# Kernel optimization log

Hardware: AMD Instinct MI355X
Metric: run time of the kernel (lower is better)

The kernel has to match this reference:

```python
import jax, jax.numpy as jnp
import numpy as np

IMAGE_SIZE = 256
NUM_FACES = 4096
NEAR = 0.1
FAR = 100.0
DRAW_BACKSIDE = False
EPS = 1e-8
CHUNK = 128  # faces processed per scan step (memory/compute tradeoff)


def setup_inputs() -> dict:
    key = jax.random.key(0)
    u = jax.random.uniform(key, (1, NUM_FACES, 3, 3), dtype=jnp.float32)  # fill=rand
    xy = u[..., :2] * 2.0 - 1.0          # screen coords in [-1, 1]
    z = u[..., 2:] * 20.0 + 1.0          # depths in [1, 21], inside (near, far)
    # shrink triangles toward their centroid -> realistic small screen-space triangles
    center = jnp.mean(xy, axis=2, keepdims=True)
    xy = center + (xy - center) * 0.15
    faces = jnp.concatenate([xy, z], axis=-1)  # [B, F, 3, 3]
    return {"faces": faces}


def _rasterize(faces):
    """Z-buffer triangle rasterization. Returns (depth_map, face_index_map).
    Matches the CUDA 'safe' kernel: per pixel, loop faces; point-in-triangle via
    same-sign edge functions; perspective-correct depth 1/zp = sum(w_i / z_i);
    keep the closest face with zp in (near, far); -1 where nothing is drawn.
    Faces are scanned in chunks to avoid materializing [B, F, S, S]."""
    B, F = faces.shape[0], faces.shape[1]
    S = IMAGE_SIZE
    ax = jnp.arange(S, dtype=jnp.float32)
    # pixel centers in normalized coords: p = (2*i + 1 - S) / S
    yp = (2.0 * ax + 1.0 - S) / S
    xp = (2.0 * ax + 1.0 - S) / S
    YP = yp[None, None, :, None]   # [1,1,S,1]
    XP = xp[None, None, None, :]   # [1,1,1,S]

    n_chunks = F // CHUNK
    fc = faces.reshape(B, n_chunks, CHUNK, 3, 3).transpose(1, 0, 2, 3, 4)  # [n,B,C,3,3]
    bases = jnp.arange(n_chunks, dtype=jnp.int32) * CHUNK

    def body(carry, inp):
        best_depth, best_face = carry          # [B,S,S] each
        fchunk, base = inp                     # [B,C,3,3], scalar face offset
        def vtx(k, c):
            return fchunk[:, :, k, c][..., None, None]  # [B,C,1,1]
        x0, y0, z0 = vtx(0, 0), vtx(0, 1), vtx(0, 2)
        x1, y1, z1 = vtx(1, 0), vtx(1, 1), vtx(1, 2)
        x2, y2, z2 = vtx(2, 0), vtx(2, 1), vtx(2, 2)

        # edge functions (unnormalized barycentric weights), [B,C,S,S]
        w0 = (YP - y1) * (x2 - x1) - (XP - x1) * (y2 - y1)
        w1 = (YP - y2) * (x0 - x2) - (XP - x2) * (y0 - y2)
        w2 = (YP - y0) * (x1 - x0) - (XP - x0) * (y1 - y0)
        inside = (w0 * w1 > 0) & (w1 * w2 > 0)  # strictly same sign -> inside

        w_sum = w0 + w1 + w2                    # sign encodes winding order
        facing = jnp.ones_like(inside) if DRAW_BACKSIDE else (w_sum > 0)

        # perspective-correct depth: zp = 1 / sum((w_i / w_sum) / z_i)
        denom = w0 / z0 + w1 / z1 + w2 / z2
        denom = jnp.where(jnp.abs(denom) > EPS, denom, EPS)
        zp = w_sum / denom

        valid = inside & facing & (NEAR < zp) & (zp < FAR)
        depth = jnp.where(valid, zp, FAR)       # [B,C,S,S]

        chunk_depth = jnp.min(depth, axis=1)            # [B,S,S]
        chunk_idx = jnp.argmin(depth, axis=1)
        update = chunk_depth < best_depth               # strict '<' like the CUDA loop
        best_depth = jnp.where(update, chunk_depth, best_depth)
        best_face = jnp.where(update, (base + chunk_idx).astype(jnp.int32), best_face)
        return (best_depth, best_face), None

    init = (jnp.full((B, S, S), FAR, jnp.float32),
            jnp.full((B, S, S), -1, jnp.int32))
    (best_depth, best_face), _ = jax.lax.scan(body, init, (fc, bases))
    return best_depth, best_face


def reference(faces):
    _, face_index_map = _rasterize(faces)
    return face_index_map  # [B, S, S] int32, -1 where no face covers the pixel
```

## Files before the change

### kernel.cpp

```cpp
#include <hip/hip_runtime.h>

#define S 256
#define NF 4096
#define TILE 16
#define HTILE 8
#define NT 1024
#define SLICES 8
#define CAPC 512
#define NEARF 0.1f
#define FARF 100.0f
#define EPSF 1e-8f

__global__ __launch_bounds__(NT, 8) void raster_tile(const float* __restrict__ faces,
                                                     int* __restrict__ out) {
    __shared__ float4 s_cand[CAPC][4];
    __shared__ unsigned long long s_key[NT];
    __shared__ int s_cnt;

    const int bx = blockIdx.x;
    const int tile = bx & 255;
    const int half = bx >> 8;
    const int tx0 = (tile & (S / TILE - 1)) * TILE;
    const int ty0 = (tile / (S / TILE)) * TILE + half * HTILE;

    const int pix = threadIdx.x & 127;
    const int slice = threadIdx.x >> 7;
    const int px = tx0 + (pix & (TILE - 1));
    const int py = ty0 + (pix >> 4);
    const float xp = (2.0f * px + 1.0f - 256.0f) * (1.0f / 256.0f);
    const float yp = (2.0f * py + 1.0f - 256.0f) * (1.0f / 256.0f);

    const float cxlo = (2.0f * tx0 + 1.0f - 256.0f) * (1.0f / 256.0f) - 1e-5f;
    const float cxhi = (2.0f * (tx0 + TILE - 1) + 1.0f - 256.0f) * (1.0f / 256.0f) + 1e-5f;
    const float cylo = (2.0f * ty0 + 1.0f - 256.0f) * (1.0f / 256.0f) - 1e-5f;
    const float cyhi = (2.0f * (ty0 + HTILE - 1) + 1.0f - 256.0f) * (1.0f / 256.0f) + 1e-5f;

    if (threadIdx.x == 0) s_cnt = 0;
    __syncthreads();

#pragma unroll
    for (int g = 0; g < 2; ++g) {
        float4 A[2], B[2];
        float Cz[2];
#pragma unroll
        for (int i = 0; i < 2; ++i) {
            const int f = g * 2048 + i * 1024 + (int)threadIdx.x;
            const float* p = faces + (size_t)f * 9;
            A[i] = *(const float4*)p;
            B[i] = *(const float4*)(p + 4);
            Cz[i] = p[8];
        }
#pragma unroll
        for (int i = 0; i < 2; ++i) {
            const float x0 = A[i].x, y0 = A[i].y, x1 = A[i].w;
            const float y1 = B[i].x, x2 = B[i].z, y2 = B[i].w;
            const float bxmin = fminf(x0, fminf(x1, x2));
            const float bxmax = fmaxf(x0, fmaxf(x1, x2));
            const float bymin = fminf(y0, fminf(y1, y2));
            const float bymax = fmaxf(y0, fmaxf(y1, y2));
            bool hit = (bxmax >= cxlo) && (bxmin <= cxhi) &&
                       (bymax >= cylo) && (bymin <= cyhi);
            const float dx21 = __fsub_rn(x2, x1), dy21 = __fsub_rn(y2, y1);
            const float dx02 = __fsub_rn(x0, x2), dy02 = __fsub_rn(y0, y2);
            const float dx10 = __fsub_rn(x1, x0), dy10 = __fsub_rn(y1, y0);
            if (hit) {
                const float a2 = __fsub_rn(
                    __fmul_rn(__fsub_rn(x1, x0), __fsub_rn(y2, y0)),
                    __fmul_rn(__fsub_rn(x2, x0), __fsub_rn(y1, y0)));
                hit = (a2 > -1e-4f);
            }
            if (hit) {
                const int f = g * 2048 + i * 1024 + (int)threadIdx.x;
                const int slot = atomicAdd(&s_cnt, 1);
                if (slot < CAPC) {
                    s_cand[slot][0] = A[i];
                    s_cand[slot][1] = B[i];
                    s_cand[slot][2] =
                        make_float4(Cz[i], __int_as_float(f), dx21, dy21);
                    s_cand[slot][3] = make_float4(dx02, dy02, dx10, dy10);
                }
            }
        }
    }
    __syncthreads();

    float bestd = FARF;
    int bestf = 0x7fffffff;

    const int n = s_cnt;
    if (n <= CAPC) {
        for (int i = slice; i < n; i += SLICES) {
            const float4 a = s_cand[i][0];
            const float4 b = s_cand[i][1];
            const float4 c = s_cand[i][2];
            const float4 d = s_cand[i][3];
            const float X0 = a.x, Y0 = a.y, Z0 = a.z, X1 = a.w;
            const float Y1 = b.x, Z1 = b.y, X2 = b.z, Y2 = b.w;
            const float Z2 = c.x;
            const int f = __float_as_int(c.y);
            const float w0 = __fsub_rn(__fmul_rn(__fsub_rn(yp, Y1), c.z),
                                       __fmul_rn(__fsub_rn(xp, X1), c.w));
            const float w1 = __fsub_rn(__fmul_rn(__fsub_rn(yp, Y2), d.x),
                                       __fmul_rn(__fsub_rn(xp, X2), d.y));
            const float w2 = __fsub_rn(__fmul_rn(__fsub_rn(yp, Y0), d.z),
                                       __fmul_rn(__fsub_rn(xp, X0), d.w));
            const bool inside = (__fmul_rn(w0, w1) > 0.0f) && (__fmul_rn(w1, w2) > 0.0f);
            const float wsum = __fadd_rn(__fadd_rn(w0, w1), w2);
            if (inside && (wsum > 0.0f)) {
                float denom = __fadd_rn(__fadd_rn(__fdiv_rn(w0, Z0), __fdiv_rn(w1, Z1)),
                                        __fdiv_rn(w2, Z2));
                denom = (fabsf(denom) > EPSF) ? denom : EPSF;
                const float zp = __fdiv_rn(wsum, denom);
                if ((zp > NEARF) && (zp < FARF)) {
                    if (zp < bestd || (zp == bestd && f < bestf)) {
                        bestd = zp;
                        bestf = f;
                    }
                }
            }
        }
    } else {
        for (int i = slice; i < NF; i += SLICES) {
            const float* p = faces + (size_t)i * 9;
            const float X0 = p[0], Y0 = p[1], Z0 = p[2];
            const float X1 = p[3], Y1 = p[4], Z1 = p[5];
            const float X2 = p[6], Y2 = p[7], Z2 = p[8];
            const float w0 = __fsub_rn(__fmul_rn(__fsub_rn(yp, Y1), __fsub_rn(X2, X1)),
                                       __fmul_rn(__fsub_rn(xp, X1), __fsub_rn(Y2, Y1)));
            const float w1 = __fsub_rn(__fmul_rn(__fsub_rn(yp, Y2), __fsub_rn(X0, X2)),
                                       __fmul_rn(__fsub_rn(xp, X2), __fsub_rn(Y0, Y2)));
            const float w2 = __fsub_rn(__fmul_rn(__fsub_rn(yp, Y0), __fsub_rn(X1, X0)),
                                       __fmul_rn(__fsub_rn(xp, X0), __fsub_rn(Y1, Y0)));
            const bool inside = (__fmul_rn(w0, w1) > 0.0f) && (__fmul_rn(w1, w2) > 0.0f);
            const float wsum = __fadd_rn(__fadd_rn(w0, w1), w2);
            if (inside && (wsum > 0.0f)) {
                float denom = __fadd_rn(__fadd_rn(__fdiv_rn(w0, Z0), __fdiv_rn(w1, Z1)),
                                        __fdiv_rn(w2, Z2));
                denom = (fabsf(denom) > EPSF) ? denom : EPSF;
                const float zp = __fdiv_rn(wsum, denom);
                if ((zp > NEARF) && (zp < FARF)) {
                    if (zp < bestd || (zp == bestd && i < bestf)) {
                        bestd = zp;
                        bestf = i;
                    }
                }
            }
        }
    }

    s_key[threadIdx.x] =
        ((unsigned long long)__float_as_uint(bestd) << 32) | (unsigned int)bestf;
    __syncthreads();
    if (threadIdx.x < 128) {
        unsigned long long k = s_key[threadIdx.x];
#pragma unroll
        for (int s = 1; s < SLICES; ++s) {
            const unsigned long long ks = s_key[threadIdx.x + 128 * s];
            k = ks < k ? ks : k;
        }
        const float dd = __uint_as_float((unsigned int)(k >> 32));
        const int fi = (int)(unsigned int)k;
        const int opx = tx0 + (threadIdx.x & (TILE - 1));
        const int opy = ty0 + (threadIdx.x >> 4);
        out[opy * S + opx] = (dd < FARF) ? fi : -1;
    }
}

extern "C" void kernel_launch(void* const* d_in, const int* in_sizes, int n_in,
                              void* d_out, int out_size, void* d_ws, size_t ws_size,
                              hipStream_t stream) {
    const float* faces = (const float*)d_in[0];
    int* out = (int*)d_out;
    hipLaunchKernelGGL(raster_tile, dim3(2 * (S / TILE) * (S / TILE)), dim3(NT), 0,
                       stream, faces, out);
}
```

Measured before the change: 25.87 us.

## Bin faces into per-tile lists in a separate pass before rendering

Adds a binning kernel that culls back-facing faces, computes each face's pixel bounding box, and appends a precomputed record to global per-half-tile lists using atomics. The render kernel then copies only its own list into shared memory, so the 512 blocks no longer each read and test all 4096 faces. This brings in a memset and a second kernel launch with global atomics and workspace traffic. The per-list capacity also shrinks to 256, and overflowing lists fall back to the full face loop.

```diff
diff --git a/kernel.cpp b/kernel.cpp
--- a/kernel.cpp
+++ b/kernel.cpp
@@ -4,24 +4,86 @@
 #define NF 4096
 #define TILE 16
 #define HTILE 8
+#define NLISTS 512
+#define CAPC 256
 #define NT 1024
 #define SLICES 8
-#define CAPC 512
 #define NEARF 0.1f
 #define FARF 100.0f
 #define EPSF 1e-8f
 
-__global__ __launch_bounds__(NT, 8) void raster_tile(const float* __restrict__ faces,
+#define WS_REC_OFF 4096
+
+__global__ __launch_bounds__(64) void bin_faces(const float* __restrict__ faces,
+                                                int* __restrict__ count,
+                                                float4* __restrict__ rec) {
+    const int f = blockIdx.x * 64 + (int)threadIdx.x;
+    const float* p = faces + (size_t)f * 9;
+    const float4 A = *(const float4*)p;
+    const float4 B = *(const float4*)(p + 4);
+    const float z2 = p[8];
+    const float x0 = A.x, y0 = A.y, x1 = A.w;
+    const float y1 = B.x, x2 = B.z, y2 = B.w;
+
+    const float a2 = __fsub_rn(__fmul_rn(__fsub_rn(x1, x0), __fsub_rn(y2, y0)),
+                               __fmul_rn(__fsub_rn(x2, x0), __fsub_rn(y1, y0)));
+    if (a2 <= -1e-4f) return;
+
+    const float bxmin = fminf(x0, fminf(x1, x2)) - 1e-3f;
+    const float bxmax = fmaxf(x0, fmaxf(x1, x2)) + 1e-3f;
+    const float bymin = fminf(y0, fminf(y1, y2)) - 1e-3f;
+    const float bymax = fmaxf(y0, fmaxf(y1, y2)) + 1e-3f;
+    int pxlo = (int)ceilf((256.0f * bxmin + 255.0f) * 0.5f) - 1;
+    int pxhi = (int)floorf((256.0f * bxmax + 255.0f) * 0.5f) + 1;
+    int pylo = (int)ceilf((256.0f * bymin + 255.0f) * 0.5f) - 1;
+    int pyhi = (int)floorf((256.0f * bymax + 255.0f) * 0.5f) + 1;
+    if (pxhi < 0 || pxlo > S - 1 || pyhi < 0 || pylo > S - 1) return;
+    pxlo = pxlo < 0 ? 0 : pxlo;
+    pylo = pylo < 0 ? 0 : pylo;
+    pxhi = pxhi > S - 1 ? S - 1 : pxhi;
+    pyhi = pyhi > S - 1 ? S - 1 : pyhi;
+
+    const float dx21 = __fsub_rn(x2, x1), dy21 = __fsub_rn(y2, y1);
+    const float dx02 = __fsub_rn(x0, x2), dy02 = __fsub_rn(y0, y2);
+    const float dx10 = __fsub_rn(x1, x0), dy10 = __fsub_rn(y1, y0);
+    const float4 r2 = make_float4(z2, __int_as_float(f), dx21, dy21);
+    const float4 r3 = make_float4(dx02, dy02, dx10, dy10);
+
+    for (int hy = pylo >> 3; hy <= pyhi >> 3; ++hy)
+        for (int hx = pxlo >> 4; hx <= pxhi >> 4; ++hx) {
+            const int list = hy * 16 + hx;
+            const int slot = atomicAdd(&count[list], 1);
+            if (slot < CAPC) {
+                float4* d = rec + ((size_t)list * CAPC + slot) * 4;
+                d[0] = A;
+                d[1] = B;
+                d[2] = r2;
+                d[3] = r3;
+            }
+        }
+}
+
+__global__ __launch_bounds__(NT, 8) void render_half(const int* __restrict__ count,
+                                                     const float4* __restrict__ rec,
+                                                     const float* __restrict__ faces,
                                                      int* __restrict__ out) {
     __shared__ float4 s_cand[CAPC][4];
     __shared__ unsigned long long s_key[NT];
-    __shared__ int s_cnt;
 
     const int bx = blockIdx.x;
     const int tile = bx & 255;
     const int half = bx >> 8;
     const int tx0 = (tile & (S / TILE - 1)) * TILE;
     const int ty0 = (tile / (S / TILE)) * TILE + half * HTILE;
+    const int list = (ty0 >> 3) * 16 + (tx0 >> 4);
+
+    const int nc = count[list];
+    const int n = nc < CAPC ? nc : CAPC;
+
+    const float4* src = rec + (size_t)list * CAPC * 4;
+    for (int k = threadIdx.x; k < n * 4; k += NT)
+        ((float4*)s_cand)[k] = src[k];
+    __syncthreads();
 
     const int pix = threadIdx.x & 127;
     const int slice = threadIdx.x >> 7;
@@ -30,65 +92,10 @@
     const float xp = (2.0f * px + 1.0f - 256.0f) * (1.0f / 256.0f);
     const float yp = (2.0f * py + 1.0f - 256.0f) * (1.0f / 256.0f);
 
-    const float cxlo = (2.0f * tx0 + 1.0f - 256.0f) * (1.0f / 256.0f) - 1e-5f;
-    const float cxhi = (2.0f * (tx0 + TILE - 1) + 1.0f - 256.0f) * (1.0f / 256.0f) + 1e-5f;
-    const float cylo = (2.0f * ty0 + 1.0f - 256.0f) * (1.0f / 256.0f) - 1e-5f;
-    const float cyhi = (2.0f * (ty0 + HTILE - 1) + 1.0f - 256.0f) * (1.0f / 256.0f) + 1e-5f;
-
-    if (threadIdx.x == 0) s_cnt = 0;
-    __syncthreads();
-
-#pragma unroll
-    for (int g = 0; g < 2; ++g) {
-        float4 A[2], B[2];
-        float Cz[2];
-#pragma unroll
-        for (int i = 0; i < 2; ++i) {
-            const int f = g * 2048 + i * 1024 + (int)threadIdx.x;
-            const float* p = faces + (size_t)f * 9;
-            A[i] = *(const float4*)p;
-            B[i] = *(const float4*)(p + 4);
-            Cz[i] = p[8];
-        }
-#pragma unroll
-        for (int i = 0; i < 2; ++i) {
-            const float x0 = A[i].x, y0 = A[i].y, x1 = A[i].w;
-            const float y1 = B[i].x, x2 = B[i].z, y2 = B[i].w;
-            const float bxmin = fminf(x0, fminf(x1, x2));
-            const float bxmax = fmaxf(x0, fmaxf(x1, x2));
-            const float bymin = fminf(y0, fminf(y1, y2));
-            const float bymax = fmaxf(y0, fmaxf(y1, y2));
-            bool hit = (bxmax >= cxlo) && (bxmin <= cxhi) &&
-                       (bymax >= cylo) && (bymin <= cyhi);
-            const float dx21 = __fsub_rn(x2, x1), dy21 = __fsub_rn(y2, y1);
-            const float dx02 = __fsub_rn(x0, x2), dy02 = __fsub_rn(y0, y2);
-            const float dx10 = __fsub_rn(x1, x0), dy10 = __fsub_rn(y1, y0);
-            if (hit) {
-                const float a2 = __fsub_rn(
-                    __fmul_rn(__fsub_rn(x1, x0), __fsub_rn(y2, y0)),
-                    __fmul_rn(__fsub_rn(x2, x0), __fsub_rn(y1, y0)));
-                hit = (a2 > -1e-4f);
-            }
-            if (hit) {
-                const int f = g * 2048 + i * 1024 + (int)threadIdx.x;
-                const int slot = atomicAdd(&s_cnt, 1);
-                if (slot < CAPC) {
-                    s_cand[slot][0] = A[i];
-                    s_cand[slot][1] = B[i];
-                    s_cand[slot][2] =
-                        make_float4(Cz[i], __int_as_float(f), dx21, dy21);
-                    s_cand[slot][3] = make_float4(dx02, dy02, dx10, dy10);
-                }
-            }
-        }
-    }
-    __syncthreads();
-
     float bestd = FARF;
     int bestf = 0x7fffffff;
 
-    const int n = s_cnt;
-    if (n <= CAPC) {
+    if (nc <= CAPC) {
         for (int i = slice; i < n; i += SLICES) {
             const float4 a = s_cand[i][0];
             const float4 b = s_cand[i][1];
@@ -160,8 +167,8 @@
         }
         const float dd = __uint_as_float((unsigned int)(k >> 32));
         const int fi = (int)(unsigned int)k;
-        const int opx = tx0 + (threadIdx.x & (TILE - 1));
-        const int opy = ty0 + (threadIdx.x >> 4);
+        const int opx = tx0 + ((int)threadIdx.x & (TILE - 1));
+        const int opy = ty0 + ((int)threadIdx.x >> 4);
         out[opy * S + opx] = (dd < FARF) ? fi : -1;
     }
 }
@@ -171,6 +178,12 @@
                               hipStream_t stream) {
     const float* faces = (const float*)d_in[0];
     int* out = (int*)d_out;
-    hipLaunchKernelGGL(raster_tile, dim3(2 * (S / TILE) * (S / TILE)), dim3(NT), 0,
-                       stream, faces, out);
+    int* count = (int*)d_ws;
+    float4* rec = (float4*)((char*)d_ws + WS_REC_OFF);
+
+    hipMemsetAsync(count, 0, NLISTS * sizeof(int), stream);
+    hipLaunchKernelGGL(bin_faces, dim3(NF / 64), dim3(64), 0, stream,
+                       faces, count, rec);
+    hipLaunchKernelGGL(render_half, dim3(2 * (S / TILE) * (S / TILE)), dim3(NT), 0,
+                       stream, count, rec, faces, out);
 }
```

Result: slower. 47.76 us (+84.6%).

## Split half-tile into two 16x4 quarter bins with per-quarter candidate lists

Applied to the files above, without the earlier changes.

Each 16x8 block now bins faces separately into two 16x4 sub-rows, with one shared-memory candidate list per sub-row. Each wavefront covers 64 pixels of one quarter and walks only that quarter's list, so faces outside that quarter's rows are never tested. All four face loads are also issued before the sync, and the inside test now checks three positive edge weights directly instead of multiplying pairs. The costs are a second atomic list, a halved per-list capacity (256) that makes the slow fallback path more likely, and a barycentric test that could differ from the reference on edge and zero cases.

```diff
diff --git a/kernel.cpp b/kernel.cpp
--- a/kernel.cpp
+++ b/kernel.cpp
@@ -6,16 +6,16 @@
 #define HTILE 8
 #define NT 1024
 #define SLICES 8
-#define CAPC 512
+#define CAPC 256
 #define NEARF 0.1f
 #define FARF 100.0f
 #define EPSF 1e-8f
 
 __global__ __launch_bounds__(NT, 8) void raster_tile(const float* __restrict__ faces,
                                                      int* __restrict__ out) {
-    __shared__ float4 s_cand[CAPC][4];
+    __shared__ float4 s_cand[2][CAPC][4];
     __shared__ unsigned long long s_key[NT];
-    __shared__ int s_cnt;
+    __shared__ int s_cnt[2];
 
     const int bx = blockIdx.x;
     const int tile = bx & 255;
@@ -23,61 +23,67 @@
     const int tx0 = (tile & (S / TILE - 1)) * TILE;
     const int ty0 = (tile / (S / TILE)) * TILE + half * HTILE;
 
-    const int pix = threadIdx.x & 127;
-    const int slice = threadIdx.x >> 7;
-    const int px = tx0 + (pix & (TILE - 1));
-    const int py = ty0 + (pix >> 4);
+    const int qr = (int)threadIdx.x >> 9;
+    const int slice = ((int)threadIdx.x >> 6) & 7;
+    const int lane = (int)threadIdx.x & 63;
+    const int px = tx0 + (lane & (TILE - 1));
+    const int py = ty0 + qr * 4 + (lane >> 4);
     const float xp = (2.0f * px + 1.0f - 256.0f) * (1.0f / 256.0f);
     const float yp = (2.0f * py + 1.0f - 256.0f) * (1.0f / 256.0f);
 
     const float cxlo = (2.0f * tx0 + 1.0f - 256.0f) * (1.0f / 256.0f) - 1e-5f;
     const float cxhi = (2.0f * (tx0 + TILE - 1) + 1.0f - 256.0f) * (1.0f / 256.0f) + 1e-5f;
-    const float cylo = (2.0f * ty0 + 1.0f - 256.0f) * (1.0f / 256.0f) - 1e-5f;
-    const float cyhi = (2.0f * (ty0 + HTILE - 1) + 1.0f - 256.0f) * (1.0f / 256.0f) + 1e-5f;
+    const float cylo0 = (2.0f * ty0 + 1.0f - 256.0f) * (1.0f / 256.0f) - 1e-5f;
+    const float cyhi0 = (2.0f * (ty0 + 3) + 1.0f - 256.0f) * (1.0f / 256.0f) + 1e-5f;
+    const float cylo1 = (2.0f * (ty0 + 4) + 1.0f - 256.0f) * (1.0f / 256.0f) - 1e-5f;
+    const float cyhi1 = (2.0f * (ty0 + 7) + 1.0f - 256.0f) * (1.0f / 256.0f) + 1e-5f;
 
-    if (threadIdx.x == 0) s_cnt = 0;
+    float4 A[4], B[4];
+    float Cz[4];
+#pragma unroll
+    for (int i = 0; i < 4; ++i) {
+        const float* p = faces + (size_t)(i * NT + threadIdx.x) * 9;
+        A[i] = *(const float4*)p;
+        B[i] = *(const float4*)(p + 4);
+        Cz[i] = p[8];
+    }
+    if (threadIdx.x < 2) s_cnt[threadIdx.x] = 0;
     __syncthreads();
 
 #pragma unroll
-    for (int g = 0; g < 2; ++g) {
-        float4 A[2], B[2];
-        float Cz[2];
-#pragma unroll
-        for (int i = 0; i < 2; ++i) {
-            const int f = g * 2048 + i * 1024 + (int)threadIdx.x;
-            const float* p = faces + (size_t)f * 9;
-            A[i] = *(const float4*)p;
-            B[i] = *(const float4*)(p + 4);
-            Cz[i] = p[8];
+    for (int i = 0; i < 4; ++i) {
+        const float x0 = A[i].x, y0 = A[i].y, x1 = A[i].w;
+        const float y1 = B[i].x, x2 = B[i].z, y2 = B[i].w;
+        const float bxmin = fminf(x0, fminf(x1, x2));
+        const float bxmax = fmaxf(x0, fmaxf(x1, x2));
+        const float bymin = fminf(y0, fminf(y1, y2));
+        const float bymax = fmaxf(y0, fmaxf(y1, y2));
+        bool xok = (bxmax >= cxlo) && (bxmin <= cxhi);
+        if (xok) {
+            const float a2 = __fsub_rn(
+                __fmul_rn(__fsub_rn(x1, x0), __fsub_rn(y2, y0)),
+                __fmul_rn(__fsub_rn(x2, x0), __fsub_rn(y1, y0)));
+            xok = (a2 > -1e-4f);
         }
-#pragma unroll
-        for (int i = 0; i < 2; ++i) {
-            const float x0 = A[i].x, y0 = A[i].y, x1 = A[i].w;
-            const float y1 = B[i].x, x2 = B[i].z, y2 = B[i].w;
-            const float bxmin = fminf(x0, fminf(x1, x2));
-            const float bxmax = fmaxf(x0, fmaxf(x1, x2));
-            const float bymin = fminf(y0, fminf(y1, y2));
-            const float bymax = fmaxf(y0, fmaxf(y1, y2));
-            bool hit = (bxmax >= cxlo) && (bxmin <= cxhi) &&
-                       (bymax >= cylo) && (bymin <= cyhi);
+        const bool hit0 = xok && (bymax >= cylo0) && (bymin <= cyhi0);
+        const bool hit1 = xok && (bymax >= cylo1) && (bymin <= cyhi1);
+        if (hit0 || hit1) {
             const float dx21 = __fsub_rn(x2, x1), dy21 = __fsub_rn(y2, y1);
             const float dx02 = __fsub_rn(x0, x2), dy02 = __fsub_rn(y0, y2);
             const float dx10 = __fsub_rn(x1, x0), dy10 = __fsub_rn(y1, y0);
-            if (hit) {
-                const float a2 = __fsub_rn(
-                    __fmul_rn(__fsub_rn(x1, x0), __fsub_rn(y2, y0)),
-                    __fmul_rn(__fsub_rn(x2, x0), __fsub_rn(y1, y0)));
-                hit = (a2 > -1e-4f);
-            }
-            if (hit) {
-                const int f = g * 2048 + i * 1024 + (int)threadIdx.x;
-                const int slot = atomicAdd(&s_cnt, 1);
-                if (slot < CAPC) {
-                    s_cand[slot][0] = A[i];
-                    s_cand[slot][1] = B[i];
-                    s_cand[slot][2] =
-                        make_float4(Cz[i], __int_as_float(f), dx21, dy21);
-                    s_cand[slot][3] = make_float4(dx02, dy02, dx10, dy10);
+            const int f = i * NT + (int)threadIdx.x;
+            const float4 r2 = make_float4(Cz[i], __int_as_float(f), dx21, dy21);
+            const float4 r3 = make_float4(dx02, dy02, dx10, dy10);
+#pragma unroll
+            for (int q = 0; q < 2; ++q) {
+                if (q == 0 ? hit0 : hit1) {
+                    const int slot = atomicAdd(&s_cnt[q], 1);
+                    if (slot < CAPC) {
+                        s_cand[q][slot][0] = A[i];
+                        s_cand[q][slot][1] = B[i];
+                        s_cand[q][slot][2] = r2;
+                        s_cand[q][slot][3] = r3;
+                    }
                 }
             }
         }
@@ -87,13 +93,13 @@
     float bestd = FARF;
     int bestf = 0x7fffffff;
 
-    const int n = s_cnt;
+    const int n = s_cnt[qr];
     if (n <= CAPC) {
         for (int i = slice; i < n; i += SLICES) {
-            const float4 a = s_cand[i][0];
-            const float4 b = s_cand[i][1];
-            const float4 c = s_cand[i][2];
-            const float4 d = s_cand[i][3];
+            const float4 a = s_cand[qr][i][0];
+            const float4 b = s_cand[qr][i][1];
+            const float4 c = s_cand[qr][i][2];
+            const float4 d = s_cand[qr][i][3];
             const float X0 = a.x, Y0 = a.y, Z0 = a.z, X1 = a.w;
             const float Y1 = b.x, Z1 = b.y, X2 = b.z, Y2 = b.w;
             const float Z2 = c.x;
@@ -104,9 +110,8 @@
                                        __fmul_rn(__fsub_rn(xp, X2), d.y));
             const float w2 = __fsub_rn(__fmul_rn(__fsub_rn(yp, Y0), d.z),
                                        __fmul_rn(__fsub_rn(xp, X0), d.w));
-            const bool inside = (__fmul_rn(w0, w1) > 0.0f) && (__fmul_rn(w1, w2) > 0.0f);
-            const float wsum = __fadd_rn(__fadd_rn(w0, w1), w2);
-            if (inside && (wsum > 0.0f)) {
+            if ((w0 > 0.0f) && (w1 > 0.0f) && (w2 > 0.0f)) {
+                const float wsum = __fadd_rn(__fadd_rn(w0, w1), w2);
                 float denom = __fadd_rn(__fadd_rn(__fdiv_rn(w0, Z0), __fdiv_rn(w1, Z1)),
                                         __fdiv_rn(w2, Z2));
                 denom = (fabsf(denom) > EPSF) ? denom : EPSF;
@@ -131,9 +136,8 @@
                                        __fmul_rn(__fsub_rn(xp, X2), __fsub_rn(Y0, Y2)));
             const float w2 = __fsub_rn(__fmul_rn(__fsub_rn(yp, Y0), __fsub_rn(X1, X0)),
                                        __fmul_rn(__fsub_rn(xp, X0), __fsub_rn(Y1, Y0)));
-            const bool inside = (__fmul_rn(w0, w1) > 0.0f) && (__fmul_rn(w1, w2) > 0.0f);
-            const float wsum = __fadd_rn(__fadd_rn(w0, w1), w2);
-            if (inside && (wsum > 0.0f)) {
+            if ((w0 > 0.0f) && (w1 > 0.0f) && (w2 > 0.0f)) {
+                const float wsum = __fadd_rn(__fadd_rn(w0, w1), w2);
                 float denom = __fadd_rn(__fadd_rn(__fdiv_rn(w0, Z0), __fdiv_rn(w1, Z1)),
                                         __fdiv_rn(w2, Z2));
                 denom = (fabsf(denom) > EPSF) ? denom : EPSF;
@@ -152,16 +156,19 @@
         ((unsigned long long)__float_as_uint(bestd) << 32) | (unsigned int)bestf;
     __syncthreads();
     if (threadIdx.x < 128) {
-        unsigned long long k = s_key[threadIdx.x];
+        const int mqr = (int)threadIdx.x >> 6;
+        const int ml = (int)threadIdx.x & 63;
+        const int base = mqr * 512 + ml;
+        unsigned long long k = s_key[base];
 #pragma unroll
         for (int s = 1; s < SLICES; ++s) {
-            const unsigned long long ks = s_key[threadIdx.x + 128 * s];
+            const unsigned long long ks = s_key[base + 64 * s];
             k = ks < k ? ks : k;
         }
         const float dd = __uint_as_float((unsigned int)(k >> 32));
         const int fi = (int)(unsigned int)k;
-        const int opx = tx0 + (threadIdx.x & (TILE - 1));
-        const int opy = ty0 + (threadIdx.x >> 4);
+        const int opx = tx0 + (ml & (TILE - 1));
+        const int opy = ty0 + mqr * 4 + (ml >> 4);
         out[opy * S + opx] = (dd < FARF) ? fi : -1;
     }
 }
```

Result: slower. 27.83 us (+7.6%).
